# Kernel tuning notes

Hardware: AMD Instinct MI355X
Metric: run time of the kernel (lower is better)

## Reference

```python
import jax, jax.numpy as jnp
from jax import lax
import numpy as np

T, B, C, H, L, K = 512, 32, 512, 512, 2, 2  # time, batch, in_feat, hidden, layers, kernel


def setup_inputs() -> dict:
    key = jax.random.key(0)
    k0, k1, k2 = jax.random.split(key, 3)
    x = jax.random.normal(k0, (T, B, C), dtype=jnp.float32)
    # per layer: [n_dir=2, n_gate=4 (z,f,o,i), H, Cin, K] conv weights and [2,4,H] biases
    w0 = jax.random.normal(k1, (2, 4, H, C, K), dtype=jnp.float32) * 0.05
    b0 = jnp.zeros((2, 4, H), dtype=jnp.float32)
    w1 = jax.random.normal(k2, (2, 4, H, 2 * H, K), dtype=jnp.float32) * 0.05
    b1 = jnp.zeros((2, 4, H), dtype=jnp.float32)
    return {"x": x, "w0": w0, "b0": b0, "w1": w1, "b1": b1}


def _conv(x, w, b):
    # x: [B, Cin, T], w: [H, Cin, K]; left-pad K-1 zeros == torch cat([zeros, x]) + VALID conv
    y = lax.conv_general_dilated(x, w, (1,), [(K - 1, 0)],
                                 dimension_numbers=("NCH", "OIH", "NCH"))
    return y + b[None, :, None]


def _qrnn_layer(x, W, b, reverse):
    # x: [B, Cin, T]; W: [4, H, Cin, K]; b: [4, H]
    if reverse:
        x = x[:, :, ::-1]  # note: original code does NOT flip the output back
    z = jnp.tanh(_conv(x, W[0], b[0]))
    f = jax.nn.sigmoid(_conv(x, W[1], b[1]))  # eval-mode zoneout: 1-(1-sigmoid)=sigmoid
    o = jax.nn.sigmoid(_conv(x, W[2], b[2]))
    i = jax.nn.sigmoid(_conv(x, W[3], b[3]))
    iz = i * z
    f_t = jnp.moveaxis(f, 2, 0)   # [T, B, H]
    iz_t = jnp.moveaxis(iz, 2, 0)

    def step(c, fi):
        ft, izt = fi
        c = ft * c + izt  # IFO pooling recurrence
        return c, c

    _, cs = lax.scan(step, jnp.zeros(f_t.shape[1:], f.dtype), (f_t, iz_t))
    c = jnp.moveaxis(cs, 0, 2)  # [B, H, T]
    return o * c


def _forward(x, w0, b0, w1, b1):
    h = jnp.transpose(x, (1, 2, 0))  # [T,B,C] -> [B,C,T]
    h_lasts = []
    for W, bb in ((w0, b0), (w1, b1)):
        d0 = _qrnn_layer(h, W[0], bb[0], False)
        d1 = _qrnn_layer(h, W[1], bb[1], True)
        t_last = h.shape[2] - 2  # lengths.fill_(T-1); t_last = lengths - 1 = T-2 (faithful)
        h_lasts.append(jnp.concatenate([d0[:, :, t_last], d1[:, :, 0]], axis=1))  # [B, 2H]
        h = jnp.concatenate([d0, d1], axis=1)  # [B, 2H, T]
    output = jnp.transpose(h, (2, 0, 1))  # [T, B, 2H]
    h_n = jnp.stack(h_lasts, axis=0)      # [L, B, 2H]
    return output, h_n


def reference(x, w0, b0, w1, b1):
    return _forward(x, w0, b0, w1, b1)
```

## Files before the change

kernel.cpp:

```cpp
#include <hip/hip_runtime.h>
#include <cstddef>
#include <cstdint>

#define Tn 512
#define Bn 32
#define Hn 512
static const size_t PLANE = 8388608;

typedef float f32x4 __attribute__((ext_vector_type(4)));
typedef __bf16 bf16x8 __attribute__((ext_vector_type(8)));
typedef _Float16 h2 __attribute__((ext_vector_type(2)));

__device__ __forceinline__ float sigm(float x) { return 1.0f / (1.0f + __expf(-x)); }
__device__ __forceinline__ float tanh_fast(float x) { return 2.0f / (1.0f + __expf(-2.0f * x)) - 1.0f; }
__device__ __forceinline__ unsigned short f2bf(float f) {
    unsigned int u = __float_as_uint(f);
    u += 0x7FFF + ((u >> 16) & 1);
    return (unsigned short)(u >> 16);
}


__global__ __launch_bounds__(256) void conv_x(const float* __restrict__ x,
                                              unsigned short* __restrict__ xbf) {
    const int i = blockIdx.x * 256 + threadIdx.x;
    const int c8 = i & 63;
    const int tp = (i >> 6) % 514;
    const int b  = (i >> 6) / 514;
    unsigned short v[8];
    if (tp == 0 || tp == 513) {
#pragma unroll
        for (int j = 0; j < 8; ++j) v[j] = 0;
    } else {
        const float* s = x + ((size_t)(tp - 1) * Bn + b) * 512 + c8 * 8;
#pragma unroll
        for (int j = 0; j < 8; ++j) v[j] = f2bf(s[j]);
    }
    unsigned short* d = xbf + ((size_t)b * 514 + tp) * 512 + c8 * 8;
    *(uint4*)d = *(const uint4*)v;
}

__global__ __launch_bounds__(256) void conv_w2(const float* __restrict__ w0,
                                               const float* __restrict__ w1,
                                               unsigned short* __restrict__ w0bf,
                                               unsigned short* __restrict__ w1bf) {
    int i = blockIdx.x * 256 + threadIdx.x;
    const float* src;
    unsigned short* dst;
    int Cin;
    if (i < 4194304) { src = w0; dst = w0bf; Cin = 512; }
    else { i -= 4194304; src = w1; dst = w1bf; Cin = 1024; }
    const int K = 2 * Cin;
    const int dm2 = i / K;
    const int kp = i - dm2 * K;
    const int dir = dm2 >> 11;
    const int mp = dm2 & 2047;
    const int o = mp >> 2;
    const int g = mp & 3;
    const int tap = (kp >= Cin) ? 1 : 0;
    const int c = kp - tap * Cin;
    dst[i] = f2bf(src[((((size_t)dir * 4 + g) * 512 + o) * Cin + c) * 2 + tap]);
}

__global__ __launch_bounds__(256) void zero_h1pad(unsigned short* __restrict__ h1bf) {
    const int i = blockIdx.x * 256 + threadIdx.x;
    const int c = i & 1023;
    const int b = (i >> 10) & 31;
    const int tp = (i >> 15) ? 513 : 0;
    h1bf[((size_t)b * 514 + tp) * 1024 + c] = 0;
}

template <int CIN>
__global__ __launch_bounds__(512, 2) void gate_gemm_bf16(
    const unsigned short* __restrict__ Wbf,
    const unsigned short* __restrict__ Xbf,
    const float* __restrict__ bias,
    h2* __restrict__ fiz,
    _Float16* __restrict__ osb,
    float* __restrict__ Fsum,
    float* __restrict__ Ssum)
{
    __shared__ __align__(16) unsigned char smem[131072];
    unsigned short* lds0 = (unsigned short*)smem;

    const int tid = threadIdx.x;
    const int lane = tid & 63;
    const int wave = tid >> 6;
    const int wm = wave >> 2;
    const int wn = wave & 3;
    const int n0 = blockIdx.x * 256;
    const int dir = blockIdx.y >> 3;
    const int m0 = (blockIdx.y & 7) * 256;
    const int S0 = CIN / 64;
    const int NS = 2 * S0;
    const int dstep = dir ? -CIN : CIN;

    const unsigned short* Wb = Wbf + (size_t)dir * 2048 * 2 * CIN;

    const unsigned short* pAs[4];
    const unsigned short* pBs[4];
#pragma unroll
    for (int r = 0; r < 4; ++r) {
        const int q = r * 512 + tid;
        const int row = q >> 3;
        const int j = q & 7;
        const int kk = j ^ ((row >> 1) & 7);
        pAs[r] = Wb + (size_t)(m0 + row) * (2 * CIN) + kk * 8;
        const int n = n0 + row;
        const int t = n & 511;
        const int b = n >> 9;
        const int tp0 = dir ? (513 - t) : t;
        pBs[r] = Xbf + ((size_t)b * 514 + tp0) * CIN + kk * 8;
    }

    const int jr0 = lane >> 4;
    int offA[8], offB[4];
#pragma unroll
    for (int f = 0; f < 8; ++f) {
        const int ma = wm * 128 + f * 16 + (lane & 15);
        offA[f] = ma * 64 + (jr0 ^ ((ma >> 1) & 7)) * 8;
    }
#pragma unroll
    for (int f = 0; f < 4; ++f) {
        const int nb = wn * 64 + f * 16 + (lane & 15);
        offB[f] = nb * 64 + (jr0 ^ ((nb >> 1) & 7)) * 8;
    }

    f32x4 acc[8][4] = {};

#define GL(P, D) __builtin_amdgcn_global_load_lds( \
        (const __attribute__((address_space(1))) unsigned int*)(P), \
        (__attribute__((address_space(3))) unsigned int*)(D), 16, 0, 0)

#define STAGE(ks, sel) do { \
    const int tap_ = ((ks) >= S0) ? 1 : 0; \
    const int aoff_ = tap_ * CIN + ((ks) - tap_ * S0) * 64; \
    const int boff_ = tap_ * dstep + ((ks) - tap_ * S0) * 64; \
    unsigned short* Ad_ = lds0 + (sel) * 32768 + tid * 8; \
    unsigned short* Bd_ = Ad_ + 16384; \
    GL(pAs[0] + aoff_, Ad_);          GL(pBs[0] + boff_, Bd_); \
    GL(pAs[1] + aoff_, Ad_ + 4096);   GL(pBs[1] + boff_, Bd_ + 4096); \
    GL(pAs[2] + aoff_, Ad_ + 8192);   GL(pBs[2] + boff_, Bd_ + 8192); \
    GL(pAs[3] + aoff_, Ad_ + 12288);  GL(pBs[3] + boff_, Bd_ + 12288); \
} while (0)

#define RD_A(mh, kh) do { \
    af[0] = *(const bf16x8*)&Ab[offA[(mh)*4+0] ^ ((kh)*32)]; \
    af[1] = *(const bf16x8*)&Ab[offA[(mh)*4+1] ^ ((kh)*32)]; \
    af[2] = *(const bf16x8*)&Ab[offA[(mh)*4+2] ^ ((kh)*32)]; \
    af[3] = *(const bf16x8*)&Ab[offA[(mh)*4+3] ^ ((kh)*32)]; \
} while (0)

#define RD_B(kh) do { \
    bfr[0] = *(const bf16x8*)&Bb[offB[0] ^ ((kh)*32)]; \
    bfr[1] = *(const bf16x8*)&Bb[offB[1] ^ ((kh)*32)]; \
    bfr[2] = *(const bf16x8*)&Bb[offB[2] ^ ((kh)*32)]; \
    bfr[3] = *(const bf16x8*)&Bb[offB[3] ^ ((kh)*32)]; \
} while (0)

#define MM(mh) do { \
    _Pragma("unroll") \
    for (int f_ = 0; f_ < 4; ++f_) { \
        _Pragma("unroll") \
        for (int fn_ = 0; fn_ < 4; ++fn_) \
            acc[(mh)*4+f_][fn_] = __builtin_amdgcn_mfma_f32_16x16x32_bf16( \
                af[f_], bfr[fn_], acc[(mh)*4+f_][fn_], 0, 0, 0); \
    } \
} while (0)

#define LGKM0 do { asm volatile("s_waitcnt lgkmcnt(0)" ::: "memory"); \
                   __builtin_amdgcn_sched_barrier(0); } while (0)

    STAGE(0, 0);
    asm volatile("s_waitcnt vmcnt(0)" ::: "memory");
    __builtin_amdgcn_s_barrier();

#pragma unroll 2
    for (int s = 0; s < NS; ++s) {
        asm volatile("" ::: "memory");
        const unsigned short* Ab = lds0 + (s & 1) * 32768;
        const unsigned short* Bb = Ab + 16384;
        bf16x8 af[4], bfr[4];
        const bool pre = (s + 1 < NS);
        if (pre) STAGE(s + 1, (s & 1) ^ 1);
        RD_B(0); RD_A(0, 0);
        __builtin_amdgcn_s_barrier();
        LGKM0;
        __builtin_amdgcn_s_setprio(1); MM(0); __builtin_amdgcn_s_setprio(0);
        __builtin_amdgcn_s_barrier();
        RD_A(1, 0);
        __builtin_amdgcn_s_barrier();
        LGKM0;
        __builtin_amdgcn_s_setprio(1); MM(1); __builtin_amdgcn_s_setprio(0);
        __builtin_amdgcn_s_barrier();
        RD_B(1); RD_A(0, 1);
        __builtin_amdgcn_s_barrier();
        LGKM0;
        __builtin_amdgcn_s_setprio(1); MM(0); __builtin_amdgcn_s_setprio(0);
        __builtin_amdgcn_s_barrier();
        RD_A(1, 1);
        __builtin_amdgcn_s_barrier();
        LGKM0;
        __builtin_amdgcn_s_setprio(1); MM(1); __builtin_amdgcn_s_setprio(0);
        if (pre) asm volatile("s_waitcnt vmcnt(0)" ::: "memory");
        __builtin_amdgcn_s_barrier();
    }
#undef GL
#undef STAGE
#undef RD_A
#undef RD_B
#undef MM
#undef LGKM0

    const int q4 = lane >> 4;
    const int o0 = (blockIdx.y & 7) * 64;
    const float* bb = bias + dir * 2048;
    h2* Lfiz = (h2*)smem;
    _Float16* Los = (_Float16*)(smem + 69632);
#pragma unroll
    for (int fm = 0; fm < 8; ++fm) {
        const int ol = wm * 32 + fm * 4 + q4;
        const int o = o0 + ol;
        const float Bz = bb[o];
        const float Bf = bb[512 + o];
        const float Bo = bb[1024 + o];
        const float Bi = bb[1536 + o];
#pragma unroll
        for (int fn = 0; fn < 4; ++fn) {
            f32x4 v = acc[fm][fn];
            const float fg = sigm(v.y + Bf);
            const float iz = sigm(v.w + Bi) * tanh_fast(v.x + Bz);
            const float og = sigm(v.z + Bo);
            const int nl = wn * 64 + fn * 16 + (lane & 15);
            h2 p; p.x = (_Float16)fg; p.y = (_Float16)iz;
            Lfiz[nl * 68 + ol] = p;
            Los[nl * 72 + ol] = (_Float16)og;
        }
    }
    __syncthreads();
    h2* fz = fiz + (size_t)dir * PLANE;
    _Float16* ob = osb + (size_t)dir * PLANE;
#pragma unroll
    for (int l = 0; l < 8; ++l) {
        const int idx = l * 512 + tid;
        const int row = idx >> 4;
        const int col = idx & 15;
        uint4 v = *(const uint4*)((const unsigned char*)smem + row * 272 + col * 16);
        ((uint4*)(fz + (size_t)(n0 + row) * 512 + o0))[col] = v;
    }
#pragma unroll
    for (int l = 0; l < 4; ++l) {
        const int idx = l * 512 + tid;
        const int row = idx >> 3;
        const int col = idx & 7;
        uint4 v = *(const uint4*)((const unsigned char*)smem + 69632 + row * 144 + col * 16);
        ((uint4*)(ob + (size_t)(n0 + row) * 512 + o0))[col] = v;
    }
    if (tid < 256) {
        const int ol = tid & 63;
        const int ch = tid >> 6;
        float F = 1.0f, S = 0.0f;
#pragma unroll
        for (int tt = 0; tt < 64; ++tt) {
            const h2 v = Lfiz[(ch * 64 + tt) * 68 + ol];
            const float fv = (float)v.x;
            F *= fv;
            S = fv * S + (float)v.y;
        }
        const int b = n0 >> 9;
        const int chg = ((n0 & 511) >> 6) + ch;
        const int o = o0 + ol;
        const int sidx = dir * 131072 + chg * 16384 + b * 512 + o;
        Fsum[sidx] = F;
        Ssum[sidx] = S;
    }
}


__global__ __launch_bounds__(256) void scan_B(
    const float* __restrict__ Fsum, const float* __restrict__ Ssum,
    float* __restrict__ cstart)
{
    const int i = blockIdx.x * 256 + threadIdx.x;
    const int base = (i >> 14) * 131072 + (i & 16383);
    float c = 0.0f;
    for (int ch = 0; ch < 8; ++ch) {
        cstart[base + ch * 16384] = c;
        c = Fsum[base + ch * 16384] * c + Ssum[base + ch * 16384];
    }
}

__global__ __launch_bounds__(256) void scan_C(
    const h2* __restrict__ fiz, const _Float16* __restrict__ osb,
    const float* __restrict__ cstart, float* __restrict__ out,
    unsigned short* __restrict__ h1bf,
    float* __restrict__ hn, int isLayer2)
{
    const int idx = blockIdx.x * 256 + threadIdx.x;
    const int dir = idx >> 17;
    const int rem = idx & 131071;
    const int o = rem & 511;
    const int b = (rem >> 9) & 31;
    const int chunk = rem >> 14;
    const int dirH = dir * 512;
    float c = cstart[idx];
    const h2* fz = fiz + (size_t)dir * PLANE;
    const _Float16* ob = osb + (size_t)dir * PLANE;
    const int tbase = chunk * 64;
    for (int tt = 0; tt < 64; ++tt) {
        const int t = tbase + tt;
        const size_t idxg = ((size_t)(b * 512 + t)) * 512 + o;
        const h2 v = fz[idxg];
        const float f = (float)v.x;
        const float iz = (float)v.y;
        const float os = (float)ob[idxg];
        c = f * c + iz;
        const float outv = os * c;
        if (isLayer2) {
            out[((size_t)t * Bn + b) * 1024 + dirH + o] = outv;
        } else {
            h1bf[((size_t)b * 514 + (t + 1)) * 1024 + dirH + o] = f2bf(outv);
        }
        const bool isLast = (dir == 0) ? (t == Tn - 2) : (t == 0);
        if (isLast) hn[(size_t)b * 1024 + dirH + o] = outv;
    }
}

extern "C" void kernel_launch(void* const* d_in, const int* in_sizes, int n_in,
                              void* d_out, int out_size, void* d_ws, size_t ws_size,
                              hipStream_t stream) {
    const float* x  = (const float*)d_in[0];
    const float* w0 = (const float*)d_in[1];
    const float* b0 = (const float*)d_in[2];
    const float* w1 = (const float*)d_in[3];
    const float* b1 = (const float*)d_in[4];
    float* out = (float*)d_out;
    float* ws = (float*)d_ws;

    h2* fiz        = (h2*)ws;
    _Float16* osb  = (_Float16*)(ws + 16777216);
    float* Fsum    = ws + 16777216 + 8388608;
    float* Ssum    = Fsum + 262144;
    float* cst     = Ssum + 262144;
    unsigned short* xbf  = (unsigned short*)(cst + 262144);
    unsigned short* h1bf = xbf + (size_t)32 * 514 * 512;
    unsigned short* w0bf = h1bf + (size_t)32 * 514 * 1024;
    unsigned short* w1bf = w0bf + (size_t)2 * 2048 * 1024;
    float* hn = out + 16777216;

    conv_x<<<4112, 256, 0, stream>>>(x, xbf);
    conv_w2<<<49152, 256, 0, stream>>>(w0, w1, w0bf, w1bf);
    zero_h1pad<<<256, 256, 0, stream>>>(h1bf);

    const dim3 gg(64, 16);

    gate_gemm_bf16<512><<<gg, 512, 0, stream>>>(w0bf, xbf, b0, fiz, osb, Fsum, Ssum);
    scan_B<<<128, 256, 0, stream>>>(Fsum, Ssum, cst);
    scan_C<<<1024, 256, 0, stream>>>(fiz, osb, cst, out, h1bf, hn, 0);
    gate_gemm_bf16<1024><<<gg, 512, 0, stream>>>(w1bf, h1bf, b1, fiz, osb, Fsum, Ssum);
    scan_B<<<128, 256, 0, stream>>>(Fsum, Ssum, cst);
    scan_C<<<1024, 256, 0, stream>>>(fiz, osb, cst, out, h1bf, hn + 32768, 1);
}
```

Baseline: 745.4 us.

## Switch GEMM mainloop to four-stage K=32 LDS pipeline with deeper prefetch

The GEMM k-step shrinks from 64 to 32 and the LDS double buffer becomes a four-slot ring with three stages prefetched ahead, using partial vmcnt waits so global loads overlap more compute. The XOR swizzle is narrowed to fit the 32-wide rows. Per-iteration barrier overhead rises because there are twice as many iterations, each carrying fewer MFMAs, and LDS use stays the same.

```diff
diff --git a/kernel.cpp b/kernel.cpp
--- a/kernel.cpp
+++ b/kernel.cpp
@@ -90,26 +90,24 @@
     const int n0 = blockIdx.x * 256;
     const int dir = blockIdx.y >> 3;
     const int m0 = (blockIdx.y & 7) * 256;
-    const int S0 = CIN / 64;
-    const int NS = 2 * S0;
+    const int S32 = CIN / 32;
+    const int NS = 2 * S32;
     const int dstep = dir ? -CIN : CIN;
 
     const unsigned short* Wb = Wbf + (size_t)dir * 2048 * 2 * CIN;
 
-    const unsigned short* pAs[4];
-    const unsigned short* pBs[4];
-#pragma unroll
-    for (int r = 0; r < 4; ++r) {
-        const int q = r * 512 + tid;
-        const int row = q >> 3;
-        const int j = q & 7;
-        const int kk = j ^ ((row >> 1) & 7);
-        pAs[r] = Wb + (size_t)(m0 + row) * (2 * CIN) + kk * 8;
+    const unsigned short* pA2[2];
+    const unsigned short* pB2[2];
+#pragma unroll
+    for (int c = 0; c < 2; ++c) {
+        const int row = c * 128 + (tid >> 2);
+        const int kk = (tid & 3) ^ ((row >> 1) & 3);
+        pA2[c] = Wb + (size_t)(m0 + row) * (2 * CIN) + kk * 8;
         const int n = n0 + row;
         const int t = n & 511;
         const int b = n >> 9;
         const int tp0 = dir ? (513 - t) : t;
-        pBs[r] = Xbf + ((size_t)b * 514 + tp0) * CIN + kk * 8;
+        pB2[c] = Xbf + ((size_t)b * 514 + tp0) * CIN + kk * 8;
     }
 
     const int jr0 = lane >> 4;
@@ -117,12 +115,12 @@
 #pragma unroll
     for (int f = 0; f < 8; ++f) {
         const int ma = wm * 128 + f * 16 + (lane & 15);
-        offA[f] = ma * 64 + (jr0 ^ ((ma >> 1) & 7)) * 8;
+        offA[f] = ma * 32 + (jr0 ^ ((ma >> 1) & 3)) * 8;
     }
 #pragma unroll
     for (int f = 0; f < 4; ++f) {
         const int nb = wn * 64 + f * 16 + (lane & 15);
-        offB[f] = nb * 64 + (jr0 ^ ((nb >> 1) & 7)) * 8;
+        offB[f] = nb * 32 + (jr0 ^ ((nb >> 1) & 3)) * 8;
     }
 
     f32x4 acc[8][4] = {};
@@ -131,30 +129,27 @@
         (const __attribute__((address_space(1))) unsigned int*)(P), \
         (__attribute__((address_space(3))) unsigned int*)(D), 16, 0, 0)
 
-#define STAGE(ks, sel) do { \
-    const int tap_ = ((ks) >= S0) ? 1 : 0; \
-    const int aoff_ = tap_ * CIN + ((ks) - tap_ * S0) * 64; \
-    const int boff_ = tap_ * dstep + ((ks) - tap_ * S0) * 64; \
-    unsigned short* Ad_ = lds0 + (sel) * 32768 + tid * 8; \
-    unsigned short* Bd_ = Ad_ + 16384; \
-    GL(pAs[0] + aoff_, Ad_);          GL(pBs[0] + boff_, Bd_); \
-    GL(pAs[1] + aoff_, Ad_ + 4096);   GL(pBs[1] + boff_, Bd_ + 4096); \
-    GL(pAs[2] + aoff_, Ad_ + 8192);   GL(pBs[2] + boff_, Bd_ + 8192); \
-    GL(pAs[3] + aoff_, Ad_ + 12288);  GL(pBs[3] + boff_, Bd_ + 12288); \
+#define STAGE(ks) do { \
+    const int tap_ = ((ks) >= S32) ? 1 : 0; \
+    const int aoff_ = tap_ * CIN + ((ks) - tap_ * S32) * 32; \
+    const int boff_ = tap_ * dstep + ((ks) - tap_ * S32) * 32; \
+    unsigned short* D_ = lds0 + ((ks) & 3) * 16384 + tid * 8; \
+    GL(pA2[0] + aoff_, D_);          GL(pA2[1] + aoff_, D_ + 4096); \
+    GL(pB2[0] + boff_, D_ + 8192);   GL(pB2[1] + boff_, D_ + 12288); \
 } while (0)
 
-#define RD_A(mh, kh) do { \
-    af[0] = *(const bf16x8*)&Ab[offA[(mh)*4+0] ^ ((kh)*32)]; \
-    af[1] = *(const bf16x8*)&Ab[offA[(mh)*4+1] ^ ((kh)*32)]; \
-    af[2] = *(const bf16x8*)&Ab[offA[(mh)*4+2] ^ ((kh)*32)]; \
-    af[3] = *(const bf16x8*)&Ab[offA[(mh)*4+3] ^ ((kh)*32)]; \
+#define RD_A(mh) do { \
+    af[0] = *(const bf16x8*)&Ab[offA[(mh)*4+0]]; \
+    af[1] = *(const bf16x8*)&Ab[offA[(mh)*4+1]]; \
+    af[2] = *(const bf16x8*)&Ab[offA[(mh)*4+2]]; \
+    af[3] = *(const bf16x8*)&Ab[offA[(mh)*4+3]]; \
 } while (0)
 
-#define RD_B(kh) do { \
-    bfr[0] = *(const bf16x8*)&Bb[offB[0] ^ ((kh)*32)]; \
-    bfr[1] = *(const bf16x8*)&Bb[offB[1] ^ ((kh)*32)]; \
-    bfr[2] = *(const bf16x8*)&Bb[offB[2] ^ ((kh)*32)]; \
-    bfr[3] = *(const bf16x8*)&Bb[offB[3] ^ ((kh)*32)]; \
+#define RD_B() do { \
+    bfr[0] = *(const bf16x8*)&Bb[offB[0]]; \
+    bfr[1] = *(const bf16x8*)&Bb[offB[1]]; \
+    bfr[2] = *(const bf16x8*)&Bb[offB[2]]; \
+    bfr[3] = *(const bf16x8*)&Bb[offB[3]]; \
 } while (0)
 
 #define MM(mh) do { \
@@ -170,38 +165,29 @@
 #define LGKM0 do { asm volatile("s_waitcnt lgkmcnt(0)" ::: "memory"); \
                    __builtin_amdgcn_sched_barrier(0); } while (0)
 
-    STAGE(0, 0);
-    asm volatile("s_waitcnt vmcnt(0)" ::: "memory");
+    STAGE(0); STAGE(1); STAGE(2);
+    asm volatile("s_waitcnt vmcnt(8)" ::: "memory");
     __builtin_amdgcn_s_barrier();
 
-#pragma unroll 2
+#pragma unroll 4
     for (int s = 0; s < NS; ++s) {
         asm volatile("" ::: "memory");
-        const unsigned short* Ab = lds0 + (s & 1) * 32768;
-        const unsigned short* Bb = Ab + 16384;
+        const unsigned short* Ab = lds0 + (s & 3) * 16384;
+        const unsigned short* Bb = Ab + 8192;
         bf16x8 af[4], bfr[4];
-        const bool pre = (s + 1 < NS);
-        if (pre) STAGE(s + 1, (s & 1) ^ 1);
-        RD_B(0); RD_A(0, 0);
+        RD_B(); RD_A(0);
+        if (s + 3 < NS) STAGE(s + 3);
         __builtin_amdgcn_s_barrier();
         LGKM0;
         __builtin_amdgcn_s_setprio(1); MM(0); __builtin_amdgcn_s_setprio(0);
         __builtin_amdgcn_s_barrier();
-        RD_A(1, 0);
+        RD_A(1);
         __builtin_amdgcn_s_barrier();
         LGKM0;
         __builtin_amdgcn_s_setprio(1); MM(1); __builtin_amdgcn_s_setprio(0);
-        __builtin_amdgcn_s_barrier();
-        RD_B(1); RD_A(0, 1);
-        __builtin_amdgcn_s_barrier();
-        LGKM0;
-        __builtin_amdgcn_s_setprio(1); MM(0); __builtin_amdgcn_s_setprio(0);
-        __builtin_amdgcn_s_barrier();
-        RD_A(1, 1);
-        __builtin_amdgcn_s_barrier();
-        LGKM0;
-        __builtin_amdgcn_s_setprio(1); MM(1); __builtin_amdgcn_s_setprio(0);
-        if (pre) asm volatile("s_waitcnt vmcnt(0)" ::: "memory");
+        if (s + 3 < NS)      { asm volatile("s_waitcnt vmcnt(8)" ::: "memory"); }
+        else if (s + 2 < NS) { asm volatile("s_waitcnt vmcnt(4)" ::: "memory"); }
+        else if (s + 1 < NS) { asm volatile("s_waitcnt vmcnt(0)" ::: "memory"); }
         __builtin_amdgcn_s_barrier();
     }
 #undef GL
```

After: 642.6 us. 13.8% less time.
